# Optimization experiments

Hardware: AMD Instinct MI355X
Metric: run time of the kernel (lower is better)

The kernel has to match this reference:

```python
import jax, jax.numpy as jnp
import numpy as np
from jax import lax

CAP = 15.0
EPS = 1e-6

def _rmsnorm(x, w):
    xf = x.astype(jnp.float32)
    var = jnp.mean(xf * xf, axis=-1, keepdims=True)
    return w * (xf * lax.rsqrt(var + EPS)).astype(x.dtype)

def _softcap_sigmoid(x):
    return jax.nn.sigmoid(CAP * jnp.tanh(x / CAP))

def setup_inputs() -> dict:
    key = jax.random.key(0)
    ks = jax.random.split(key, 4)
    B, S, D, P = 8, 2048, 1024, 1365
    x = jax.random.normal(ks[0], (B, S, D), dtype=jnp.float32)
    h0 = jnp.zeros((B, P), dtype=jnp.float32)
    ln_weight = jnp.ones((D,), dtype=jnp.float32)
    gate_w = jax.random.normal(ks[1], (3 * P, D), dtype=jnp.float32) * 0.02
    cell_w = jax.random.normal(ks[2], (P, D), dtype=jnp.float32) * 0.02
    out_w = jax.random.normal(ks[3], (D, P), dtype=jnp.float32) * 0.02
    return {"x": x, "h0": h0, "ln_weight": ln_weight, "gate_w": gate_w,
            "cell_w": cell_w, "out_w": out_w}

def reference(x, h0, ln_weight, gate_w, cell_w, out_w):
    B, S, D = x.shape
    P = cell_w.shape[0]
    residual = x
    xn = _rmsnorm(x, ln_weight)
    # gates: [B,S,3P] -> [B,S,3,P]
    gates = jnp.einsum('bsd,gd->bsg', xn, gate_w).reshape(B, S, 3, P)
    g = _softcap_sigmoid(gates)
    i_gate, f_gate, o_gate = g[:, :, 0], g[:, :, 1], g[:, :, 2]
    c_input = jnp.einsum('bsd,pd->bsp', xn, cell_w)
    # sequential sLSTM recurrence over time via scan; xs are time-major [S,B,P]
    xs = (jnp.swapaxes(c_input, 0, 1), jnp.swapaxes(i_gate, 0, 1),
          jnp.swapaxes(f_gate, 0, 1), jnp.swapaxes(o_gate, 0, 1))
    def step(h, ts):
        c_t, i_t, f_t, o_t = ts
        h = f_t * h + i_t * jnp.tanh(c_t)
        return h, o_t * jnp.tanh(h)
    h_final, ys = lax.scan(step, h0, xs)
    output = jnp.swapaxes(ys, 0, 1)  # [B,S,P]
    out = residual + jnp.einsum('bsp,dp->bsd', output, out_w)
    return (out, h_final)
```

## Files before the change

kernel.cpp:

```cpp
#include <hip/hip_runtime.h>
#include <hip/hip_bf16.h>
#include <cstdint>

#define B_   8
#define S_   2048
#define D_   1024
#define P_   1365
#define M_   (B_*S_)
#define KP   1408
#define NGCP (4*KP)
#define CHUNK 32
#define CMAX (S_/CHUNK)

typedef __attribute__((ext_vector_type(8))) short bf16x8;
typedef __attribute__((ext_vector_type(4))) float f32x4;

__device__ __forceinline__ float fast_rcp(float x) {
  return __builtin_amdgcn_rcpf(x);
}
__device__ __forceinline__ float fast_tanh(float x) {
  float e = __expf(2.0f * x);
  return 1.0f - 2.0f * fast_rcp(e + 1.0f);
}
__device__ __forceinline__ float softcap_sig(float x) {
  float u = x * (1.0f / 15.0f);
  float z = -x + x * u * u * (1.0f / 3.0f);
  return fast_rcp(1.0f + __expf(z));
}
__device__ __forceinline__ float bf2f(unsigned short u) {
  union { float f; unsigned int i; } x; x.i = ((unsigned)u) << 16; return x.f;
}
__device__ __forceinline__ unsigned short f2bf(float f) {
  __hip_bfloat16 h = __float2bfloat16(f);
  return *reinterpret_cast<unsigned short*>(&h);
}
__device__ __forceinline__ void gload_lds16(const void* g, void* l) {
  __builtin_amdgcn_global_load_lds(
      (const __attribute__((address_space(1))) uint32_t*)g,
      (__attribute__((address_space(3))) uint32_t*)l,
      16, 0, 0);
}

#define BAR do { asm volatile("" ::: "memory"); __builtin_amdgcn_s_barrier(); \
                 asm volatile("" ::: "memory"); } while (0)

__global__ void k_prep_wgc(const float* __restrict__ gate_w,
                           const float* __restrict__ cell_w,
                           __hip_bfloat16* __restrict__ wgc) {
  int gid = blockIdx.x * blockDim.x + threadIdx.x;
  int idx = gid * 4;
  int r = idx >> 10, c = idx & 1023;
  int g = r / KP;
  int rr = r - g * KP;
  float4 v;
  if (rr < P_) {
    if (g < 3) v = *(const float4*)(gate_w + (size_t)(g * P_ + rr) * D_ + c);
    else       v = *(const float4*)(cell_w + (size_t)rr * D_ + c);
  } else v = make_float4(0.f, 0.f, 0.f, 0.f);
  __hip_bfloat16* dst = wgc + idx;
  dst[0] = __float2bfloat16(v.x); dst[1] = __float2bfloat16(v.y);
  dst[2] = __float2bfloat16(v.z); dst[3] = __float2bfloat16(v.w);
}

__global__ void k_prep_wout(const float* __restrict__ out_w,
                            __hip_bfloat16* __restrict__ wout) {
  int gid = blockIdx.x * blockDim.x + threadIdx.x;
  int idx = gid * 4;
  int d = idx / KP, p = idx - d * KP;
  __hip_bfloat16* dst = wout + idx;
  #pragma unroll
  for (int j = 0; j < 4; ++j) {
    int pp = p + j;
    float v = (pp < P_) ? out_w[(size_t)d * P_ + pp] : 0.f;
    dst[j] = __float2bfloat16(v);
  }
}

__global__ __launch_bounds__(256) void k_rmsnorm(const float* __restrict__ x,
                                                 const float* __restrict__ w,
                                                 __hip_bfloat16* __restrict__ xn) {
  __shared__ float red[4];
  int m = blockIdx.x;
  int tid = threadIdx.x;
  float4 v = ((const float4*)(x + (size_t)m * D_))[tid];
  float ss = v.x * v.x + v.y * v.y + v.z * v.z + v.w * v.w;
  #pragma unroll
  for (int off = 32; off > 0; off >>= 1) ss += __shfl_down(ss, off);
  if ((tid & 63) == 0) red[tid >> 6] = ss;
  __syncthreads();
  float tot = red[0] + red[1] + red[2] + red[3];
  float scale = rsqrtf(tot * (1.0f / (float)D_) + 1e-6f);
  float4 wv = ((const float4*)w)[tid];
  __hip_bfloat16* o = xn + (size_t)m * D_ + tid * 4;
  o[0] = __float2bfloat16(v.x * scale * wv.x);
  o[1] = __float2bfloat16(v.y * scale * wv.y);
  o[2] = __float2bfloat16(v.z * scale * wv.z);
  o[3] = __float2bfloat16(v.w * scale * wv.w);
}

template<int LDK, int KT, bool GATES>
__global__ __launch_bounds__(512, 2) void k_gemm256(
    const __hip_bfloat16* __restrict__ A,
    const __hip_bfloat16* __restrict__ Bw,
    __hip_bfloat16* __restrict__ pi, __hip_bfloat16* __restrict__ pf,
    __hip_bfloat16* __restrict__ po, __hip_bfloat16* __restrict__ ptc,
    const float* __restrict__ xres, float* __restrict__ out,
    int s0, int sc_shift, int NBY) {
  __shared__ __align__(16) __hip_bfloat16 lA[2][256 * 64];
  __shared__ __align__(16) __hip_bfloat16 lB[2][256 * 64];
  const int tid = threadIdx.x;
  const int lane = tid & 63;
  const int wid = tid >> 6;
  const int wm = wid >> 2, wn = wid & 3;
  const int lr = lane & 15, lg = lane >> 4;
  const int bx = blockIdx.x / NBY;
  const int by = blockIdx.x % NBY;
  const int rl0 = by * 256;
  const int col0 = bx * 256;
  const int scm = (1 << sc_shift) - 1;

  auto grow_of = [&](int rl) -> size_t {
    int bb = rl >> sc_shift;
    return (size_t)bb * S_ + s0 + (rl & scm);
  };

  auto stage_half = [&](int t, int arr, int h) {
    const int buf = t & 1;
    const int k0 = t * 64;
    #pragma unroll
    for (int l = 0; l < 2; ++l) {
      int s = l * 512 + tid;
      int r = h * 128 + (s >> 3);
      int c = (s & 7) * 8;
      int csrc = c ^ ((r & 7) << 3);
      if (arr == 0) {
        size_t ar = GATES ? grow_of(rl0 + r) : (size_t)(rl0 + r);
        gload_lds16(A + ar * LDK + k0 + csrc, &lA[buf][r * 64 + c]);
      } else {
        gload_lds16(Bw + (size_t)(col0 + r) * LDK + k0 + csrc, &lB[buf][r * 64 + c]);
      }
    }
  };

  auto rdA = [&](int buf, int mi, int ks) -> bf16x8 {
    int R = wm * 128 + mi * 16 + lr;
    int ec = (ks * 32 + lg * 8) ^ ((R & 7) << 3);
    return *(const bf16x8*)&lA[buf][R * 64 + ec];
  };
  auto rdB = [&](int buf, int ni, int ks) -> bf16x8 {
    int R = wn * 64 + ni * 16 + lr;
    int ec = (ks * 32 + lg * 8) ^ ((R & 7) << 3);
    return *(const bf16x8*)&lB[buf][R * 64 + ec];
  };

  const f32x4 zero = {0.f, 0.f, 0.f, 0.f};
  f32x4 acc[8][4];
  #pragma unroll
  for (int i = 0; i < 8; ++i)
    #pragma unroll
    for (int j = 0; j < 4; ++j) acc[i][j] = zero;

  stage_half(0, 1, 0); stage_half(0, 1, 1);
  stage_half(0, 0, 0); stage_half(0, 0, 1);
  stage_half(1, 1, 0); stage_half(1, 1, 1);
  asm volatile("s_waitcnt vmcnt(4)" ::: "memory");
  BAR;

  const int ITERS = KT / 2;
  for (int i = 0; i < ITERS; ++i) {
    const bool lastIt = (i == ITERS - 1);
    const int o = 2 * i + 1, t2 = 2 * i + 2, t3 = 2 * i + 3;
    bf16x8 af[4][2], bfr[4][2];

    #pragma unroll
    for (int mi = 0; mi < 4; ++mi) { af[mi][0] = rdA(0, mi, 0); af[mi][1] = rdA(0, mi, 1); }
    #pragma unroll
    for (int ni = 0; ni < 2; ++ni) { bfr[ni][0] = rdB(0, ni, 0); bfr[ni][1] = rdB(0, ni, 1); }
    stage_half(o, 0, 0);
    BAR;
    __builtin_amdgcn_s_setprio(1);
    #pragma unroll
    for (int mi = 0; mi < 4; ++mi)
      #pragma unroll
      for (int ni = 0; ni < 2; ++ni)
        #pragma unroll
        for (int ks = 0; ks < 2; ++ks)
          acc[mi][ni] = __builtin_amdgcn_mfma_f32_16x16x32_bf16(af[mi][ks], bfr[ni][ks], acc[mi][ni], 0, 0, 0);
    __builtin_amdgcn_s_setprio(0);
    BAR;
    #pragma unroll
    for (int ni = 2; ni < 4; ++ni) { bfr[ni][0] = rdB(0, ni, 0); bfr[ni][1] = rdB(0, ni, 1); }
    stage_half(o, 0, 1);
    BAR;
    __builtin_amdgcn_s_setprio(1);
    #pragma unroll
    for (int mi = 0; mi < 4; ++mi)
      #pragma unroll
      for (int ni = 2; ni < 4; ++ni)
        #pragma unroll
        for (int ks = 0; ks < 2; ++ks)
          acc[mi][ni] = __builtin_amdgcn_mfma_f32_16x16x32_bf16(af[mi][ks], bfr[ni][ks], acc[mi][ni], 0, 0, 0);
    __builtin_amdgcn_s_setprio(0);
    BAR;
    #pragma unroll
    for (int mi = 0; mi < 4; ++mi) { af[mi][0] = rdA(0, mi + 4, 0); af[mi][1] = rdA(0, mi + 4, 1); }
    if (t2 < KT) stage_half(t2, 1, 0);
    BAR;
    __builtin_amdgcn_s_setprio(1);
    #pragma unroll
    for (int mi = 0; mi < 4; ++mi)
      #pragma unroll
      for (int ni = 2; ni < 4; ++ni)
        #pragma unroll
        for (int ks = 0; ks < 2; ++ks)
          acc[mi + 4][ni] = __builtin_amdgcn_mfma_f32_16x16x32_bf16(af[mi][ks], bfr[ni][ks], acc[mi + 4][ni], 0, 0, 0);
    __builtin_amdgcn_s_setprio(0);
    BAR;
    if (t2 < KT) stage_half(t2, 1, 1);
    BAR;
    __builtin_amdgcn_s_setprio(1);
    #pragma unroll
    for (int mi = 0; mi < 4; ++mi)
      #pragma unroll
      for (int ni = 0; ni < 2; ++ni)
        #pragma unroll
        for (int ks = 0; ks < 2; ++ks)
          acc[mi + 4][ni] = __builtin_amdgcn_mfma_f32_16x16x32_bf16(af[mi][ks], bfr[ni][ks], acc[mi + 4][ni], 0, 0, 0);
    __builtin_amdgcn_s_setprio(0);
    if (lastIt) { asm volatile("s_waitcnt vmcnt(0)" ::: "memory"); }
    else        { asm volatile("s_waitcnt vmcnt(4)" ::: "memory"); }
    BAR;

    #pragma unroll
    for (int mi = 0; mi < 4; ++mi) { af[mi][0] = rdA(1, mi, 0); af[mi][1] = rdA(1, mi, 1); }
    #pragma unroll
    for (int ni = 0; ni < 2; ++ni) { bfr[ni][0] = rdB(1, ni, 0); bfr[ni][1] = rdB(1, ni, 1); }
    if (t2 < KT) stage_half(t2, 0, 0);
    BAR;
    __builtin_amdgcn_s_setprio(1);
    #pragma unroll
    for (int mi = 0; mi < 4; ++mi)
      #pragma unroll
      for (int ni = 0; ni < 2; ++ni)
        #pragma unroll
        for (int ks = 0; ks < 2; ++ks)
          acc[mi][ni] = __builtin_amdgcn_mfma_f32_16x16x32_bf16(af[mi][ks], bfr[ni][ks], acc[mi][ni], 0, 0, 0);
    __builtin_amdgcn_s_setprio(0);
    BAR;
    #pragma unroll
    for (int ni = 2; ni < 4; ++ni) { bfr[ni][0] = rdB(1, ni, 0); bfr[ni][1] = rdB(1, ni, 1); }
    if (t2 < KT) stage_half(t2, 0, 1);
    BAR;
    __builtin_amdgcn_s_setprio(1);
    #pragma unroll
    for (int mi = 0; mi < 4; ++mi)
      #pragma unroll
      for (int ni = 2; ni < 4; ++ni)
        #pragma unroll
        for (int ks = 0; ks < 2; ++ks)
          acc[mi][ni] = __builtin_amdgcn_mfma_f32_16x16x32_bf16(af[mi][ks], bfr[ni][ks], acc[mi][ni], 0, 0, 0);
    __builtin_amdgcn_s_setprio(0);
    BAR;
    #pragma unroll
    for (int mi = 0; mi < 4; ++mi) { af[mi][0] = rdA(1, mi + 4, 0); af[mi][1] = rdA(1, mi + 4, 1); }
    if (t3 < KT) stage_half(t3, 1, 0);
    BAR;
    __builtin_amdgcn_s_setprio(1);
    #pragma unroll
    for (int mi = 0; mi < 4; ++mi)
      #pragma unroll
      for (int ni = 2; ni < 4; ++ni)
        #pragma unroll
        for (int ks = 0; ks < 2; ++ks)
          acc[mi + 4][ni] = __builtin_amdgcn_mfma_f32_16x16x32_bf16(af[mi][ks], bfr[ni][ks], acc[mi + 4][ni], 0, 0, 0);
    __builtin_amdgcn_s_setprio(0);
    BAR;
    if (t3 < KT) stage_half(t3, 1, 1);
    BAR;
    __builtin_amdgcn_s_setprio(1);
    #pragma unroll
    for (int mi = 0; mi < 4; ++mi)
      #pragma unroll
      for (int ni = 0; ni < 2; ++ni)
        #pragma unroll
        for (int ks = 0; ks < 2; ++ks)
          acc[mi + 4][ni] = __builtin_amdgcn_mfma_f32_16x16x32_bf16(af[mi][ks], bfr[ni][ks], acc[mi + 4][ni], 0, 0, 0);
    __builtin_amdgcn_s_setprio(0);
    if (lastIt) { asm volatile("s_waitcnt vmcnt(0)" ::: "memory"); }
    else        { asm volatile("s_waitcnt vmcnt(4)" ::: "memory"); }
    BAR;
  }

  if (GATES) {
    #pragma unroll
    for (int ni = 0; ni < 4; ++ni) {
      int gn = col0 + wn * 64 + ni * 16 + lr;
      int g = gn / KP;
      int p = gn - g * KP;
      __hip_bfloat16* plane = (g == 0) ? pi : (g == 1) ? pf : (g == 2) ? po : ptc;
      const bool istanh = (g == 3);
      #pragma unroll
      for (int mi = 0; mi < 8; ++mi) {
        #pragma unroll
        for (int j = 0; j < 4; ++j) {
          int rl = rl0 + wm * 128 + mi * 16 + lg * 4 + j;
          float v = acc[mi][ni][j];
          float r = istanh ? fast_tanh(v) : softcap_sig(v);
          plane[(size_t)rl * KP + p] = __float2bfloat16(r);
        }
      }
    }
  } else {
    #pragma unroll
    for (int ni = 0; ni < 4; ++ni) {
      int gn = col0 + wn * 64 + ni * 16 + lr;
      #pragma unroll
      for (int mi = 0; mi < 8; ++mi) {
        #pragma unroll
        for (int j = 0; j < 4; ++j) {
          int rl = rl0 + wm * 128 + mi * 16 + lg * 4 + j;
          size_t o2 = grow_of(rl) * D_ + gn;
          out[o2] = xres[o2] + acc[mi][ni][j];
        }
      }
    }
  }
}

__global__ __launch_bounds__(256) void k_scan_p1(
    const __hip_bfloat16* __restrict__ pi, const __hip_bfloat16* __restrict__ pf,
    const __hip_bfloat16* __restrict__ ptc,
    float* __restrict__ Abuf, float* __restrict__ Bbuf, int C) {
  int t = blockIdx.x * blockDim.x + threadIdx.x;
  int p4 = t % (KP / 4);
  int rest = t / (KP / 4);
  int b = rest & 7;
  int c = rest >> 3;
  int p = p4 * 4;
  size_t base = ((size_t)b * C * CHUNK + (size_t)c * CHUNK) * KP + p;
  float4 Aa = make_float4(1.f, 1.f, 1.f, 1.f);
  float4 Bc = make_float4(0.f, 0.f, 0.f, 0.f);
  #pragma unroll 8
  for (int sl = 0; sl < CHUNK; ++sl) {
    size_t idx = base + (size_t)sl * KP;
    ushort4 vf = *reinterpret_cast<const ushort4*>(pf + idx);
    ushort4 vi = *reinterpret_cast<const ushort4*>(pi + idx);
    ushort4 vt = *reinterpret_cast<const ushort4*>(ptc + idx);
    float f0 = bf2f(vf.x), f1 = bf2f(vf.y), f2 = bf2f(vf.z), f3 = bf2f(vf.w);
    Aa.x *= f0; Aa.y *= f1; Aa.z *= f2; Aa.w *= f3;
    Bc.x = f0 * Bc.x + bf2f(vi.x) * bf2f(vt.x);
    Bc.y = f1 * Bc.y + bf2f(vi.y) * bf2f(vt.y);
    Bc.z = f2 * Bc.z + bf2f(vi.z) * bf2f(vt.z);
    Bc.w = f3 * Bc.w + bf2f(vi.w) * bf2f(vt.w);
  }
  size_t o = ((size_t)c * B_ + b) * KP + p;
  *reinterpret_cast<float4*>(Abuf + o) = Aa;
  *reinterpret_cast<float4*>(Bbuf + o) = Bc;
}

__global__ __launch_bounds__(256) void k_scan_p2(
    const float* __restrict__ Abuf, const float* __restrict__ Bbuf,
    const float* __restrict__ h_in, float* __restrict__ carry,
    float* __restrict__ h_out, int C) {
  int t = blockIdx.x * blockDim.x + threadIdx.x;
  int b = t / KP;
  int p = t - b * KP;
  float h = (p < P_) ? h_in[(size_t)b * P_ + p] : 0.f;
  #pragma unroll 8
  for (int c = 0; c < C; ++c) {
    size_t o = ((size_t)c * B_ + b) * KP + p;
    carry[o] = h;
    h = Abuf[o] * h + Bbuf[o];
  }
  if (p < P_) h_out[(size_t)b * P_ + p] = h;
}

__global__ __launch_bounds__(256) void k_scan_p3(
    const __hip_bfloat16* __restrict__ pi, const __hip_bfloat16* __restrict__ pf,
    const __hip_bfloat16* __restrict__ po, __hip_bfloat16* __restrict__ ptc,
    const float* __restrict__ carry, int C) {
  int t = blockIdx.x * blockDim.x + threadIdx.x;
  int p4 = t % (KP / 4);
  int rest = t / (KP / 4);
  int b = rest & 7;
  int c = rest >> 3;
  int p = p4 * 4;
  float4 h4 = *reinterpret_cast<const float4*>(carry + ((size_t)c * B_ + b) * KP + p);
  size_t base = ((size_t)b * C * CHUNK + (size_t)c * CHUNK) * KP + p;
  #pragma unroll 4
  for (int sl = 0; sl < CHUNK; ++sl) {
    size_t idx = base + (size_t)sl * KP;
    ushort4 vf = *reinterpret_cast<const ushort4*>(pf + idx);
    ushort4 vi = *reinterpret_cast<const ushort4*>(pi + idx);
    ushort4 vo = *reinterpret_cast<const ushort4*>(po + idx);
    ushort4 vt = *reinterpret_cast<const ushort4*>(ptc + idx);
    h4.x = bf2f(vf.x) * h4.x + bf2f(vi.x) * bf2f(vt.x);
    h4.y = bf2f(vf.y) * h4.y + bf2f(vi.y) * bf2f(vt.y);
    h4.z = bf2f(vf.z) * h4.z + bf2f(vi.z) * bf2f(vt.z);
    h4.w = bf2f(vf.w) * h4.w + bf2f(vi.w) * bf2f(vt.w);
    ushort4 y;
    y.x = f2bf(bf2f(vo.x) * fast_tanh(h4.x));
    y.y = f2bf(bf2f(vo.y) * fast_tanh(h4.y));
    y.z = f2bf(bf2f(vo.z) * fast_tanh(h4.z));
    y.w = f2bf(bf2f(vo.w) * fast_tanh(h4.w));
    *reinterpret_cast<ushort4*>(ptc + idx) = y;
  }
}

extern "C" void kernel_launch(void* const* d_in, const int* in_sizes, int n_in,
                              void* d_out, int out_size, void* d_ws, size_t ws_size,
                              hipStream_t stream) {
  const float* x      = (const float*)d_in[0];
  const float* h0     = (const float*)d_in[1];
  const float* lnw    = (const float*)d_in[2];
  const float* gate_w = (const float*)d_in[3];
  const float* cell_w = (const float*)d_in[4];
  const float* out_w  = (const float*)d_in[5];
  float* out  = (float*)d_out;
  float* hfin = out + (size_t)M_ * D_;

  size_t off = 0;
  char* ws = (char*)d_ws;
  __hip_bfloat16* xn   = (__hip_bfloat16*)(ws + off); off += (size_t)M_ * D_ * 2;
  __hip_bfloat16* wgc  = (__hip_bfloat16*)(ws + off); off += (size_t)NGCP * D_ * 2;
  __hip_bfloat16* wout = (__hip_bfloat16*)(ws + off); off += (size_t)D_ * KP * 2;
  float* hbuf          = (float*)(ws + off);          off += (size_t)B_ * P_ * 4;
  float* Abuf          = (float*)(ws + off);          off += (size_t)CMAX * B_ * KP * 4;
  float* Bbuf          = (float*)(ws + off);          off += (size_t)CMAX * B_ * KP * 4;
  float* carry         = (float*)(ws + off);          off += (size_t)CMAX * B_ * KP * 4;
  off = (off + 255) & ~(size_t)255;

  int nchunks = 1;
  while (nchunks < 16) {
    size_t planes = 4ull * B_ * (S_ / nchunks) * KP * 2;
    if (off + planes <= ws_size) break;
    nchunks <<= 1;
  }
  const int Sc = S_ / nchunks;
  const int C = Sc / CHUNK;
  int sc_shift = 0;
  while ((1 << sc_shift) < Sc) ++sc_shift;
  __hip_bfloat16* pi  = (__hip_bfloat16*)(ws + off); off += (size_t)B_ * Sc * KP * 2;
  __hip_bfloat16* pf  = (__hip_bfloat16*)(ws + off); off += (size_t)B_ * Sc * KP * 2;
  __hip_bfloat16* po  = (__hip_bfloat16*)(ws + off); off += (size_t)B_ * Sc * KP * 2;
  __hip_bfloat16* ptc = (__hip_bfloat16*)(ws + off); off += (size_t)B_ * Sc * KP * 2;

  k_prep_wgc<<<dim3(NGCP * D_ / 1024), dim3(256), 0, stream>>>(gate_w, cell_w, wgc);
  k_prep_wout<<<dim3(D_ * KP / 1024), dim3(256), 0, stream>>>(out_w, wout);
  k_rmsnorm<<<dim3(M_), dim3(256), 0, stream>>>(x, lnw, xn);

  for (int c = 0; c < nchunks; ++c) {
    int s0 = c * Sc;
    const int NBY = B_ * Sc / 256;
    k_gemm256<D_, D_/64, true><<<dim3((NGCP / 256) * NBY), dim3(512), 0, stream>>>(
        xn, wgc, pi, pf, po, ptc, nullptr, nullptr, s0, sc_shift, NBY);
    int np1 = B_ * C * (KP / 4);
    k_scan_p1<<<dim3(np1 / 256), dim3(256), 0, stream>>>(pi, pf, ptc, Abuf, Bbuf, C);
    k_scan_p2<<<dim3(B_ * KP / 256), dim3(256), 0, stream>>>(
        Abuf, Bbuf, (c == 0) ? h0 : hbuf, carry,
        (c == nchunks - 1) ? hfin : hbuf, C);
    k_scan_p3<<<dim3(np1 / 256), dim3(256), 0, stream>>>(pi, pf, po, ptc, carry, C);
    k_gemm256<KP, KP/64, false><<<dim3((D_ / 256) * NBY), dim3(512), 0, stream>>>(
        ptc, wout, nullptr, nullptr, nullptr, nullptr, x, out, s0, sc_shift, NBY);
  }
}
```

Measured before the change: 479.5 us.

## Stage gate GEMM epilogue through LDS for vectorized stores and swizzle block order

The gate GEMM epilogue now writes activated bf16 results into a shared-memory tile, then each thread stores 16-byte vectors to the gate planes, replacing scattered 2-byte global stores. The LDS arrays are merged into a single raw buffer so the epilogue can reuse it. Block indices are also remapped with a stride-8 permutation, likely to group tiles by XCD for better L2 reuse. This adds a barrier and LDS round trip, and relies on KP being a multiple of 8 so vector chunks never straddle gate planes.

```diff
diff --git a/kernel.cpp b/kernel.cpp
--- a/kernel.cpp
+++ b/kernel.cpp
@@ -106,15 +106,20 @@
     __hip_bfloat16* __restrict__ po, __hip_bfloat16* __restrict__ ptc,
     const float* __restrict__ xres, float* __restrict__ out,
     int s0, int sc_shift, int NBY) {
-  __shared__ __align__(16) __hip_bfloat16 lA[2][256 * 64];
-  __shared__ __align__(16) __hip_bfloat16 lB[2][256 * 64];
+  __shared__ __align__(16) char smem[131072];
+  __hip_bfloat16* ldsA = (__hip_bfloat16*)smem;
+  __hip_bfloat16* ldsB = (__hip_bfloat16*)(smem + 65536);
   const int tid = threadIdx.x;
   const int lane = tid & 63;
   const int wid = tid >> 6;
   const int wm = wid >> 2, wn = wid & 3;
   const int lr = lane & 15, lg = lane >> 4;
-  const int bx = blockIdx.x / NBY;
-  const int by = blockIdx.x % NBY;
+
+  const int NX = gridDim.x / NBY;
+  const int cpx = gridDim.x >> 3;
+  const int w2 = (blockIdx.x & 7) * cpx + (blockIdx.x >> 3);
+  const int by = w2 / NX;
+  const int bx = w2 - by * NX;
   const int rl0 = by * 256;
   const int col0 = bx * 256;
   const int scm = (1 << sc_shift) - 1;
@@ -135,9 +140,10 @@
       int csrc = c ^ ((r & 7) << 3);
       if (arr == 0) {
         size_t ar = GATES ? grow_of(rl0 + r) : (size_t)(rl0 + r);
-        gload_lds16(A + ar * LDK + k0 + csrc, &lA[buf][r * 64 + c]);
+        gload_lds16(A + ar * LDK + k0 + csrc, ldsA + buf * 16384 + r * 64 + c);
       } else {
-        gload_lds16(Bw + (size_t)(col0 + r) * LDK + k0 + csrc, &lB[buf][r * 64 + c]);
+        gload_lds16(Bw + (size_t)(col0 + r) * LDK + k0 + csrc,
+                    ldsB + buf * 16384 + r * 64 + c);
       }
     }
   };
@@ -145,12 +151,12 @@
   auto rdA = [&](int buf, int mi, int ks) -> bf16x8 {
     int R = wm * 128 + mi * 16 + lr;
     int ec = (ks * 32 + lg * 8) ^ ((R & 7) << 3);
-    return *(const bf16x8*)&lA[buf][R * 64 + ec];
+    return *(const bf16x8*)&ldsA[buf * 16384 + R * 64 + ec];
   };
   auto rdB = [&](int buf, int ni, int ks) -> bf16x8 {
     int R = wn * 64 + ni * 16 + lr;
     int ec = (ks * 32 + lg * 8) ^ ((R & 7) << 3);
-    return *(const bf16x8*)&lB[buf][R * 64 + ec];
+    return *(const bf16x8*)&ldsB[buf * 16384 + R * 64 + ec];
   };
 
   const f32x4 zero = {0.f, 0.f, 0.f, 0.f};
@@ -292,23 +298,35 @@
   }
 
   if (GATES) {
+    __hip_bfloat16* Ct = (__hip_bfloat16*)smem;
     #pragma unroll
     for (int ni = 0; ni < 4; ++ni) {
-      int gn = col0 + wn * 64 + ni * 16 + lr;
-      int g = gn / KP;
-      int p = gn - g * KP;
-      __hip_bfloat16* plane = (g == 0) ? pi : (g == 1) ? pf : (g == 2) ? po : ptc;
+      int cc = wn * 64 + ni * 16 + lr;
+      int g = (col0 + wn * 64 + ni * 16) / KP;
       const bool istanh = (g == 3);
       #pragma unroll
       for (int mi = 0; mi < 8; ++mi) {
         #pragma unroll
         for (int j = 0; j < 4; ++j) {
-          int rl = rl0 + wm * 128 + mi * 16 + lg * 4 + j;
+          int rr = wm * 128 + mi * 16 + lg * 4 + j;
           float v = acc[mi][ni][j];
-          float r = istanh ? fast_tanh(v) : softcap_sig(v);
-          plane[(size_t)rl * KP + p] = __float2bfloat16(r);
+          Ct[rr * 256 + cc] = __float2bfloat16(istanh ? fast_tanh(v) : softcap_sig(v));
         }
       }
+    }
+    __syncthreads();
+    #pragma unroll
+    for (int it = 0; it < 16; ++it) {
+      int idx = it * 512 + tid;
+      int rr = idx >> 5;
+      int ck = idx & 31;
+      int gn8 = col0 + ck * 8;
+      int g = gn8 / KP;
+      int p = gn8 - g * KP;
+      __hip_bfloat16* plane = (g == 0) ? pi : (g == 1) ? pf : (g == 2) ? po : ptc;
+      size_t rl = (size_t)(rl0 + rr);
+      *reinterpret_cast<float4*>(&plane[rl * KP + p]) =
+          *reinterpret_cast<const float4*>(&Ct[rr * 256 + ck * 8]);
     }
   } else {
     #pragma unroll
```

New measurement: 518.2 us. 8.1% more time.
